# Optimization experiments

Measured on AMD Instinct MI355X. Metric: run time of the kernel, lower is better.

Reference implementation:

```python
import jax, jax.numpy as jnp
import numpy as np

S_CUR, S_MEM, B, D, DFF, L, H = 4096, 16384, 1, 256, 2048, 4, 1
EPS = 1e-5


def _ln(x, w, b):
    mu = x.mean(-1, keepdims=True)
    var = ((x - mu) ** 2).mean(-1, keepdims=True)
    return (x - mu) * jax.lax.rsqrt(var + EPS) * w + b


def _mha(q_in, k_in, v_in, w_qkv, b_qkv, w_o, b_o):
    # torch nn.MultiheadAttention convention: y = x @ W.T + b
    q = q_in @ w_qkv[0].T + b_qkv[0]
    k = k_in @ w_qkv[1].T + b_qkv[1]
    v = v_in @ w_qkv[2].T + b_qkv[2]
    Bq, Sq, _ = q.shape
    Sk = k.shape[1]
    hd = D // H
    q = q.reshape(Bq, Sq, H, hd)
    k = k.reshape(Bq, Sk, H, hd)
    v = v.reshape(Bq, Sk, H, hd)
    scores = jnp.einsum('bqhd,bkhd->bhqk', q, k) / jnp.sqrt(jnp.asarray(hd, q.dtype))
    attn = jax.nn.softmax(scores, axis=-1)
    out = jnp.einsum('bhqk,bkhd->bqhd', attn, v).reshape(Bq, Sq, D)
    return out @ w_o.T + b_o


def setup_inputs() -> dict:
    key = jax.random.key(0)
    ks = jax.random.split(key, 20)
    p = lambda i, shape: 0.02 * jax.random.normal(ks[i], shape, dtype=jnp.float32)
    return {
        'curr': jax.random.normal(ks[0], (S_CUR, B, D), jnp.float32),
        'memory': jax.random.normal(ks[1], (S_MEM, B, D), jnp.float32),
        'curr_pos': jax.random.normal(ks[2], (S_CUR, B, D), jnp.float32),
        'memory_pos': jax.random.normal(ks[3], (S_MEM, B, D), jnp.float32),
        'sa_w_qkv': p(4, (L, 3, D, D)), 'sa_b_qkv': p(5, (L, 3, D)),
        'sa_w_o': p(6, (L, D, D)), 'sa_b_o': p(7, (L, D)),
        'ca_w_qkv': p(8, (L, 3, D, D)), 'ca_b_qkv': p(9, (L, 3, D)),
        'ca_w_o': p(10, (L, D, D)), 'ca_b_o': p(11, (L, D)),
        'ln1_w': jnp.ones((L, D)), 'ln1_b': jnp.zeros((L, D)),
        'ln2_w': jnp.ones((L, D)), 'ln2_b': jnp.zeros((L, D)),
        'ln3_w': jnp.ones((L, D)), 'ln3_b': jnp.zeros((L, D)),
        'mlp_w1': p(12, (L, DFF, D)), 'mlp_b1': p(13, (L, DFF)),
        'mlp_w2': p(14, (L, D, DFF)), 'mlp_b2': p(15, (L, D)),
        'norm_w': jnp.ones((D,)), 'norm_b': jnp.zeros((D,)),
    }


def reference(curr, memory, curr_pos, memory_pos,
              sa_w_qkv, sa_b_qkv, sa_w_o, sa_b_o,
              ca_w_qkv, ca_b_qkv, ca_w_o, ca_b_o,
              ln1_w, ln1_b, ln2_w, ln2_b, ln3_w, ln3_b,
              mlp_w1, mlp_b1, mlp_w2, mlp_b2, norm_w, norm_b):
    # pos_enc_at_input: output = curr + 0.1 * curr_pos (seq-first (S, B, D))
    x = curr + 0.1 * curr_pos
    # batch_first: transpose to (B, S, D) for the layers
    x = jnp.transpose(x, (1, 0, 2))
    mem = jnp.transpose(memory, (1, 0, 2))
    mem_k = mem + jnp.transpose(memory_pos, (1, 0, 2))  # pos added to cross-attn keys
    for l in range(L):
        # pre-norm self-attention (no query_pos at self-attn in SAM2 default)
        t2 = _ln(x, ln1_w[l], ln1_b[l])
        x = x + _mha(t2, t2, t2, sa_w_qkv[l], sa_b_qkv[l], sa_w_o[l], sa_b_o[l])
        # pre-norm cross-attention to memory (keys carry memory_pos, values do not)
        t2 = _ln(x, ln2_w[l], ln2_b[l])
        x = x + _mha(t2, mem_k, mem, ca_w_qkv[l], ca_b_qkv[l], ca_w_o[l], ca_b_o[l])
        # pre-norm ReLU MLP
        t2 = _ln(x, ln3_w[l], ln3_b[l])
        x = x + jax.nn.relu(t2 @ mlp_w1[l].T + mlp_b1[l]) @ mlp_w2[l].T + mlp_b2[l]
    out = _ln(x, norm_w, norm_b)
    return jnp.transpose(out, (1, 0, 2))  # back to (S, B, D)
```

## Files before the change

### kernel.cpp

```cpp
#include <hip/hip_runtime.h>
#include <hip/hip_bf16.h>

typedef unsigned short u16;
typedef unsigned int u32;
typedef __attribute__((ext_vector_type(8))) __bf16 bf16x8;
typedef __attribute__((ext_vector_type(4))) float f32x4;
typedef __attribute__((ext_vector_type(4))) u16 u16x4;
typedef __attribute__((ext_vector_type(8))) u16 u16x8;

#define SCUR 4096
#define SMEM 16384
#define DM   256
#define DFFN 2048
#define NL   4

__device__ __forceinline__ u16 f2b(float f){
  u32 i; __builtin_memcpy(&i, &f, 4);
  u32 r = (i + 0x7fffu + ((i >> 16) & 1u)) >> 16;
  return (u16)r;
}
__device__ __forceinline__ float b2f(u16 v){
  u32 i = ((u32)v) << 16; float f; __builtin_memcpy(&f, &i, 4); return f;
}

__device__ __forceinline__ f32x4 mfma16(bf16x8 a, bf16x8 b, f32x4 c){
  return __builtin_amdgcn_mfma_f32_16x16x32_bf16(a, b, c, 0, 0, 0);
}

__device__ __forceinline__ void glds16(const u16* g, u16* l){
  __builtin_amdgcn_global_load_lds(
      (const __attribute__((address_space(1))) u32*)g,
      (__attribute__((address_space(3))) u32*)l, 16, 0, 0);
}


__global__ void axpy_k(const float* __restrict__ a, const float* __restrict__ b,
                       float s, float* __restrict__ o, int n4){
  int i = blockIdx.x * blockDim.x + threadIdx.x;
  int st = gridDim.x * blockDim.x;
  for (; i < n4; i += st){
    float4 x = ((const float4*)a)[i];
    float4 y = ((const float4*)b)[i];
    float4 r; r.x = x.x + s*y.x; r.y = x.y + s*y.y; r.z = x.z + s*y.z; r.w = x.w + s*y.w;
    ((float4*)o)[i] = r;
  }
}

__global__ void cvt_bf16_k(const float* __restrict__ a, const float* __restrict__ b,
                           u16* __restrict__ o, int n4, float s){
  int i = blockIdx.x * blockDim.x + threadIdx.x;
  int st = gridDim.x * blockDim.x;
  const bool hb = (b != nullptr);
  for (; i < n4; i += st){
    float4 x = ((const float4*)a)[i];
    if (hb){
      float4 y = ((const float4*)b)[i];
      x.x += s*y.x; x.y += s*y.y; x.z += s*y.z; x.w += s*y.w;
    }
    u16x4 r = { f2b(x.x), f2b(x.y), f2b(x.z), f2b(x.w) };
    ((u16x4*)o)[i] = r;
  }
}

template<int OUTF32>
__global__ __launch_bounds__(256) void ln_k(const float* __restrict__ X,
    const float* __restrict__ g, const float* __restrict__ b,
    void* __restrict__ out, int rows){
  int row = blockIdx.x * 4 + (threadIdx.x >> 6);
  int lane = threadIdx.x & 63;
  if (row >= rows) return;
  const float4 v = *(const float4*)(X + (size_t)row*DM + lane*4);
  float s = v.x + v.y + v.z + v.w;
  for (int off = 1; off < 64; off <<= 1) s += __shfl_xor(s, off, 64);
  float mu = s * (1.f/256.f);
  float dx = v.x-mu, dy = v.y-mu, dz = v.z-mu, dw = v.w-mu;
  float q = dx*dx + dy*dy + dz*dz + dw*dw;
  for (int off = 1; off < 64; off <<= 1) q += __shfl_xor(q, off, 64);
  float rstd = rsqrtf(q * (1.f/256.f) + 1e-5f);
  const float4 gw = *(const float4*)(g + lane*4);
  const float4 gb = *(const float4*)(b + lane*4);
  float y0 = dx*rstd*gw.x + gb.x;
  float y1 = dy*rstd*gw.y + gb.y;
  float y2 = dz*rstd*gw.z + gb.z;
  float y3 = dw*rstd*gw.w + gb.w;
  if (OUTF32){
    float4 o; o.x=y0; o.y=y1; o.z=y2; o.w=y3;
    *(float4*)((float*)out + (size_t)row*DM + lane*4) = o;
  } else {
    u16x4 o = { f2b(y0), f2b(y1), f2b(y2), f2b(y3) };
    *(u16x4*)((u16*)out + (size_t)row*DM + lane*4) = o;
  }
}

template<int EPI>
__global__ __launch_bounds__(256) void gemm_bt(
    const u16* __restrict__ A, int lda, const u16* __restrict__ W, int ldw,
    const float* __restrict__ bias, void* __restrict__ out, int ldc,
    int M, int N, int K){
  __shared__ u16 a_sm[64*40];
  __shared__ u16 b_sm[64*40];
  const int tid = threadIdx.x;
  const int lane = tid & 63;
  const int w = tid >> 6;
  const int l16 = lane & 15, lg = lane >> 4;
  const int m0 = blockIdx.y * 64;
  const int n0 = blockIdx.x * 64;
  const int wr = (w >> 1) * 32, wc = (w & 1) * 32;
  f32x4 acc[2][2] = {};
  const int srow = tid >> 2, sch = tid & 3;
  const u16* Ag = A + (size_t)(m0 + srow) * lda + sch * 8;
  const u16* Wg = W + (size_t)(n0 + srow) * ldw + sch * 8;
  u16x8 av = *(const u16x8*)(Ag);
  u16x8 wv = *(const u16x8*)(Wg);
  for (int k0 = 0; k0 < K; k0 += 32){
    __syncthreads();
    *(u16x8*)(a_sm + srow*40 + sch*8) = av;
    *(u16x8*)(b_sm + srow*40 + sch*8) = wv;
    if (k0 + 32 < K){
      av = *(const u16x8*)(Ag + k0 + 32);
      wv = *(const u16x8*)(Wg + k0 + 32);
    }
    __syncthreads();
    bf16x8 af0 = *(const bf16x8*)(a_sm + (wr      + l16)*40 + lg*8);
    bf16x8 af1 = *(const bf16x8*)(a_sm + (wr + 16 + l16)*40 + lg*8);
    bf16x8 bf0 = *(const bf16x8*)(b_sm + (wc      + l16)*40 + lg*8);
    bf16x8 bf1 = *(const bf16x8*)(b_sm + (wc + 16 + l16)*40 + lg*8);
    acc[0][0] = mfma16(af0, bf0, acc[0][0]);
    acc[0][1] = mfma16(af0, bf1, acc[0][1]);
    acc[1][0] = mfma16(af1, bf0, acc[1][0]);
    acc[1][1] = mfma16(af1, bf1, acc[1][1]);
  }
  for (int mi = 0; mi < 2; mi++)
    for (int ni = 0; ni < 2; ni++)
      for (int r = 0; r < 4; r++){
        int m = m0 + wr + mi*16 + lg*4 + r;
        int n = n0 + wc + ni*16 + l16;
        float v = acc[mi][ni][r];
        if (EPI == 3)      v += bias[m];
        else if (EPI != 4) v += bias[n];
        if (EPI == 2)      ((float*)out)[(size_t)m*ldc + n] += v;
        else if (EPI == 1) ((u16*)out)[(size_t)m*ldc + n] = f2b(v > 0.f ? v : 0.f);
        else               ((u16*)out)[(size_t)m*ldc + n] = f2b(v);
      }
}

template<int EPI>
__global__ void gemm128(
    const u16* __restrict__ A, int lda, const u16* __restrict__ W, int ldw,
    const float* __restrict__ bias, void* __restrict__ out, int ldc,
    int M, int N, int K){
  __shared__ u16 a_sm[2][128*32];
  __shared__ u16 b_sm[2][128*32];
  const int tid = threadIdx.x, lane = tid & 63, w = tid >> 6;
  const int l16 = lane & 15, lg = lane >> 4;
  const int m0 = blockIdx.y * 128, n0 = blockIdx.x * 128;
  const int wr = (w >> 1) * 64, wc = (w & 1) * 64;
  f32x4 acc[4][4] = {};
  const int c0 = w*64 + lane, c1 = c0 + 256;
  const int r0 = c0 >> 2, cc0 = c0 & 3;
  const int r1 = c1 >> 2, cc1 = c1 & 3;
  const u16* Ag0 = A + (size_t)(m0 + r0)*lda + cc0*8;
  const u16* Ag1 = A + (size_t)(m0 + r1)*lda + cc1*8;
  const u16* Wg0 = W + (size_t)(n0 + r0)*ldw + cc0*8;
  const u16* Wg1 = W + (size_t)(n0 + r1)*ldw + cc1*8;
  const int nk = K >> 5;
  glds16(Ag0, a_sm[0] + w*512);
  glds16(Ag1, a_sm[0] + w*512 + 2048);
  glds16(Wg0, b_sm[0] + w*512);
  glds16(Wg1, b_sm[0] + w*512 + 2048);
  __builtin_amdgcn_sched_barrier(0);
  for (int k = 0; k < nk; k++){
    const int cur = k & 1;
    if (k + 1 < nk){
      const int nxt = cur ^ 1;
      const int ko = (k + 1) * 32;
      glds16(Ag0 + ko, a_sm[nxt] + w*512);
      glds16(Ag1 + ko, a_sm[nxt] + w*512 + 2048);
      glds16(Wg0 + ko, b_sm[nxt] + w*512);
      glds16(Wg1 + ko, b_sm[nxt] + w*512 + 2048);
      __builtin_amdgcn_sched_barrier(0);
      asm volatile("s_waitcnt vmcnt(4)" ::: "memory");
    } else {
      asm volatile("s_waitcnt vmcnt(0)" ::: "memory");
    }
    __builtin_amdgcn_s_barrier();
    bf16x8 af[4], bf[4];
    #pragma unroll
    for (int mi = 0; mi < 4; mi++)
      af[mi] = *(const bf16x8*)(a_sm[cur] + (wr + mi*16 + l16)*32 + lg*8);
    #pragma unroll
    for (int ni = 0; ni < 4; ni++)
      bf[ni] = *(const bf16x8*)(b_sm[cur] + (wc + ni*16 + l16)*32 + lg*8);
    #pragma unroll
    for (int mi = 0; mi < 4; mi++)
      #pragma unroll
      for (int ni = 0; ni < 4; ni++)
        acc[mi][ni] = mfma16(af[mi], bf[ni], acc[mi][ni]);
    __builtin_amdgcn_s_barrier();
  }
  #pragma unroll
  for (int mi = 0; mi < 4; mi++)
    #pragma unroll
    for (int ni = 0; ni < 4; ni++)
      #pragma unroll
      for (int r = 0; r < 4; r++){
        int m = m0 + wr + mi*16 + lg*4 + r;
        int n = n0 + wc + ni*16 + l16;
        float v = acc[mi][ni][r];
        if (EPI == 1){
          v += bias[n];
          ((u16*)out)[(size_t)m*ldc + n] = f2b(v > 0.f ? v : 0.f);
        } else {
          ((u16*)out)[(size_t)m*ldc + n] = f2b(v);
        }
      }
}

template<int EXPA>
__global__ __launch_bounds__(256) void gemm_pv(
    const u16* __restrict__ A, int lda, const u16* __restrict__ W, int ldw,
    u16* __restrict__ out, int M, int K,
    float* __restrict__ lpart, float scale){
  __shared__ u16 a_sm[64*40];
  __shared__ u16 b_sm[256*40];
  const int tid = threadIdx.x, lane = tid & 63, w = tid >> 6;
  const int l16 = lane & 15, lg = lane >> 4;
  const int m0 = blockIdx.x * 64;
  const int koff = blockIdx.y * K;
  f32x4 acc[4][4] = {};
  const int srow = tid >> 2, sch = tid & 3;
  float lsum = 0.f;
  const u16* Ag = A + (size_t)(m0 + srow) * lda + sch * 8 + koff;
  const u16* Wg = W + (size_t)srow * ldw + sch * 8 + koff;
  u16x8 avX = *(const u16x8*)(Ag);
  u16x8 wv0X = *(const u16x8*)(Wg);
  u16x8 wv1X = *(const u16x8*)(Wg + (size_t)64*ldw);
  u16x8 wv2X = *(const u16x8*)(Wg + (size_t)128*ldw);
  u16x8 wv3X = *(const u16x8*)(Wg + (size_t)192*ldw);
  u16x8 avY = *(const u16x8*)(Ag + 32);
  u16x8 wv0Y = *(const u16x8*)(Wg + 32);
  u16x8 wv1Y = *(const u16x8*)(Wg + (size_t)64*ldw + 32);
  u16x8 wv2Y = *(const u16x8*)(Wg + (size_t)128*ldw + 32);
  u16x8 wv3Y = *(const u16x8*)(Wg + (size_t)192*ldw + 32);
  for (int k0 = 0; k0 < K; k0 += 64){
    u16x8 as;
    if (EXPA){
      #pragma unroll
      for (int e = 0; e < 8; e++){
        float p = __expf(b2f(avX[e]) * scale);
        lsum += p;
        as[e] = f2b(p);
      }
    } else as = avX;
    __syncthreads();
    *(u16x8*)(a_sm + srow*40 + sch*8) = as;
    *(u16x8*)(b_sm + srow*40 + sch*8) = wv0X;
    *(u16x8*)(b_sm + (srow+64)*40 + sch*8) = wv1X;
    *(u16x8*)(b_sm + (srow+128)*40 + sch*8) = wv2X;
    *(u16x8*)(b_sm + (srow+192)*40 + sch*8) = wv3X;
    if (k0 + 64 < K){
      avX  = *(const u16x8*)(Ag + k0 + 64);
      wv0X = *(const u16x8*)(Wg + k0 + 64);
      wv1X = *(const u16x8*)(Wg + (size_t)64*ldw + k0 + 64);
      wv2X = *(const u16x8*)(Wg + (size_t)128*ldw + k0 + 64);
      wv3X = *(const u16x8*)(Wg + (size_t)192*ldw + k0 + 64);
    }
    __syncthreads();
    {
      bf16x8 af[4], bf[4];
      #pragma unroll
      for (int i = 0; i < 4; i++)
        af[i] = *(const bf16x8*)(a_sm + (i*16 + l16)*40 + lg*8);
      #pragma unroll
      for (int i = 0; i < 4; i++)
        bf[i] = *(const bf16x8*)(b_sm + (w*64 + i*16 + l16)*40 + lg*8);
      #pragma unroll
      for (int mi = 0; mi < 4; mi++)
        #pragma unroll
        for (int ni = 0; ni < 4; ni++)
          acc[mi][ni] = mfma16(af[mi], bf[ni], acc[mi][ni]);
    }
    if (EXPA){
      #pragma unroll
      for (int e = 0; e < 8; e++){
        float p = __expf(b2f(avY[e]) * scale);
        lsum += p;
        as[e] = f2b(p);
      }
    } else as = avY;
    __syncthreads();
    *(u16x8*)(a_sm + srow*40 + sch*8) = as;
    *(u16x8*)(b_sm + srow*40 + sch*8) = wv0Y;
    *(u16x8*)(b_sm + (srow+64)*40 + sch*8) = wv1Y;
    *(u16x8*)(b_sm + (srow+128)*40 + sch*8) = wv2Y;
    *(u16x8*)(b_sm + (srow+192)*40 + sch*8) = wv3Y;
    if (k0 + 96 < K){
      avY  = *(const u16x8*)(Ag + k0 + 96);
      wv0Y = *(const u16x8*)(Wg + k0 + 96);
      wv1Y = *(const u16x8*)(Wg + (size_t)64*ldw + k0 + 96);
      wv2Y = *(const u16x8*)(Wg + (size_t)128*ldw + k0 + 96);
      wv3Y = *(const u16x8*)(Wg + (size_t)192*ldw + k0 + 96);
    }
    __syncthreads();
    {
      bf16x8 af[4], bf[4];
      #pragma unroll
      for (int i = 0; i < 4; i++)
        af[i] = *(const bf16x8*)(a_sm + (i*16 + l16)*40 + lg*8);
      #pragma unroll
      for (int i = 0; i < 4; i++)
        bf[i] = *(const bf16x8*)(b_sm + (w*64 + i*16 + l16)*40 + lg*8);
      #pragma unroll
      for (int mi = 0; mi < 4; mi++)
        #pragma unroll
        for (int ni = 0; ni < 4; ni++)
          acc[mi][ni] = mfma16(af[mi], bf[ni], acc[mi][ni]);
    }
  }
  if (EXPA){
    lsum += __shfl_xor(lsum, 1, 64);
    lsum += __shfl_xor(lsum, 2, 64);
    if (sch == 0) lpart[(size_t)blockIdx.y * M + m0 + srow] = lsum;
  }
  u16* op = out + (size_t)blockIdx.y * M * 256;
  #pragma unroll
  for (int mi = 0; mi < 4; mi++)
    #pragma unroll
    for (int ni = 0; ni < 4; ni++)
      #pragma unroll
      for (int r = 0; r < 4; r++){
        int m = m0 + mi*16 + lg*4 + r;
        int n = w*64 + ni*16 + l16;
        op[(size_t)m*256 + n] = f2b(acc[mi][ni][r]);
      }
}

__global__ __launch_bounds__(256) void reduce_pv_k(const u16* __restrict__ P,
    const float* __restrict__ lpart, u16* __restrict__ O, int M, int ks){
  int m = blockIdx.x, d = threadIdx.x;
  const size_t st = (size_t)M * 256;
  float s = 0.f, l = 0.f;
  for (int i = 0; i < ks; i++){
    s += b2f(P[(size_t)i*st + (size_t)m*256 + d]);
    l += lpart[(size_t)i*M + m];
  }
  O[(size_t)m*256 + d] = f2b(s / l);
}
__global__ __launch_bounds__(256) void reduce_res_k(const u16* __restrict__ P,
    const float* __restrict__ bias, float* __restrict__ X, int M, int ks){
  int m = blockIdx.x, d = threadIdx.x;
  const size_t st = (size_t)M * 256;
  float s = bias[d];
  for (int i = 0; i < ks; i++) s += b2f(P[(size_t)i*st + (size_t)m*256 + d]);
  X[(size_t)m*256 + d] += s;
}

extern "C" void kernel_launch(void* const* d_in, const int* in_sizes, int n_in,
                              void* d_out, int out_size, void* d_ws, size_t ws_size,
                              hipStream_t stream){
  (void)in_sizes; (void)n_in; (void)out_size;
  const float* curr       = (const float*)d_in[0];
  const float* memory     = (const float*)d_in[1];
  const float* curr_pos   = (const float*)d_in[2];
  const float* memory_pos = (const float*)d_in[3];
  const float* sa_w_qkv   = (const float*)d_in[4];
  const float* sa_b_qkv   = (const float*)d_in[5];
  const float* sa_w_o     = (const float*)d_in[6];
  const float* sa_b_o     = (const float*)d_in[7];
  const float* ca_w_qkv   = (const float*)d_in[8];
  const float* ca_b_qkv   = (const float*)d_in[9];
  const float* ca_w_o     = (const float*)d_in[10];
  const float* ca_b_o     = (const float*)d_in[11];
  const float* ln1_w = (const float*)d_in[12];
  const float* ln1_b = (const float*)d_in[13];
  const float* ln2_w = (const float*)d_in[14];
  const float* ln2_b = (const float*)d_in[15];
  const float* ln3_w = (const float*)d_in[16];
  const float* ln3_b = (const float*)d_in[17];
  const float* mlp_w1 = (const float*)d_in[18];
  const float* mlp_b1 = (const float*)d_in[19];
  const float* mlp_w2 = (const float*)d_in[20];
  const float* mlp_b2 = (const float*)d_in[21];
  const float* norm_w = (const float*)d_in[22];
  const float* norm_b = (const float*)d_in[23];

  char* wsp = (char*)d_ws;
  auto alloc = [&](size_t bytes)->void*{
    void* r = (void*)wsp; wsp += (bytes + 255) & ~(size_t)255; return r;
  };
  float* x     = (float*)alloc((size_t)SCUR*DM*4);
  u16*   t2b   = (u16*)  alloc((size_t)SCUR*DM*2);
  u16*   qkb   = (u16*)  alloc((size_t)SCUR*2*DM*2);
  u16*   vtsb  = (u16*)  alloc((size_t)DM*SCUR*2);
  u16*   Kb    = (u16*)  alloc((size_t)SMEM*DM*2);
  u16*   vtcb  = (u16*)  alloc((size_t)DM*SMEM*2);
  u16*   memkb = (u16*)  alloc((size_t)SMEM*DM*2);
  u16*   memb  = (u16*)  alloc((size_t)SMEM*DM*2);
  u16*   Hb    = (u16*)  alloc((size_t)SCUR*DFFN*2);
  u16*   Ppart = (u16*)  alloc((size_t)8*SCUR*DM*2);
  float* lpart = (float*)alloc((size_t)16*SCUR*4);
  u16* wb_sa_qkv = (u16*)alloc((size_t)NL*3*DM*DM*2);
  u16* wb_sa_o   = (u16*)alloc((size_t)NL*DM*DM*2);
  u16* wb_ca_qkv = (u16*)alloc((size_t)NL*3*DM*DM*2);
  u16* wb_ca_o   = (u16*)alloc((size_t)NL*DM*DM*2);
  u16* wb_m1     = (u16*)alloc((size_t)NL*DFFN*DM*2);
  u16* wb_m2     = (u16*)alloc((size_t)NL*DM*DFFN*2);

  size_t used  = (size_t)(wsp - (char*)d_ws);
  size_t avail = (ws_size > used) ? (ws_size - used) : 0;
  const size_t rowb = (size_t)SMEM * 2;
  u16* Sbuf;
  int CHc;
  if (avail >= (size_t)SCUR * rowb){
    CHc = SCUR;
    Sbuf = (u16*)alloc((size_t)SCUR * rowb);
  } else {
    size_t ch = (avail / rowb) & ~(size_t)127;
    if (ch >= 512){
      CHc = (int)(ch > SCUR ? SCUR : ch);
      Sbuf = (u16*)alloc((size_t)CHc * rowb);
    } else {
      CHc = 512;
      Sbuf = Hb;
    }
  }
  size_t scap = (size_t)CHc * rowb;
  int CHs = (int)(scap / ((size_t)SCUR*2));
  if (CHs > SCUR) CHs = SCUR;
  CHs &= ~127;
  if (CHs < 128) CHs = 128;

  u16* PVc; int ksc;
  if (Sbuf != Hb){ PVc = Hb; ksc = 16; }
  else           { PVc = Ppart; ksc = 8; }

  u16* Ob = t2b;
  u16* Qb = qkb;

  const float* nullf = nullptr;
  float* nulll = nullptr;
  const float sc = 0.0625f;

  axpy_k<<<dim3(512), dim3(256), 0, stream>>>(curr, curr_pos, 0.1f, x, SCUR*DM/4);
  cvt_bf16_k<<<dim3(1024), dim3(256), 0, stream>>>(memory, memory_pos, memkb, SMEM*DM/4, 1.0f);
  cvt_bf16_k<<<dim3(1024), dim3(256), 0, stream>>>(memory, nullf, memb, SMEM*DM/4, 0.f);
  cvt_bf16_k<<<dim3(512), dim3(256), 0, stream>>>(sa_w_qkv, nullf, wb_sa_qkv, NL*3*DM*DM/4, 0.f);
  cvt_bf16_k<<<dim3(256), dim3(256), 0, stream>>>(sa_w_o,   nullf, wb_sa_o,   NL*DM*DM/4,   0.f);
  cvt_bf16_k<<<dim3(512), dim3(256), 0, stream>>>(ca_w_qkv, nullf, wb_ca_qkv, NL*3*DM*DM/4, 0.f);
  cvt_bf16_k<<<dim3(256), dim3(256), 0, stream>>>(ca_w_o,   nullf, wb_ca_o,   NL*DM*DM/4,   0.f);
  cvt_bf16_k<<<dim3(1024), dim3(256), 0, stream>>>(mlp_w1,  nullf, wb_m1,     NL*DFFN*DM/4, 0.f);
  cvt_bf16_k<<<dim3(1024), dim3(256), 0, stream>>>(mlp_w2,  nullf, wb_m2,     NL*DM*DFFN/4, 0.f);

  const dim3 blk(256);
  for (int l = 0; l < NL; l++){
    ln_k<0><<<dim3(SCUR/4), blk, 0, stream>>>(x, ln1_w + l*DM, ln1_b + l*DM, (void*)t2b, SCUR);
    gemm_bt<0><<<dim3(512/64, SCUR/64), blk, 0, stream>>>(t2b, DM, wb_sa_qkv + (size_t)l*3*DM*DM, DM,
        sa_b_qkv + (size_t)l*3*DM, (void*)qkb, 512, SCUR, 512, DM);
    gemm_bt<3><<<dim3(SCUR/64, DM/64), blk, 0, stream>>>(wb_sa_qkv + ((size_t)l*3+2)*DM*DM, DM, t2b, DM,
        sa_b_qkv + (size_t)l*3*DM + 2*DM, (void*)vtsb, SCUR, DM, SCUR, DM);
    for (int c = 0; c < SCUR; c += CHs){
      int Mc = (SCUR - c) < CHs ? (SCUR - c) : CHs;
      gemm128<4><<<dim3(SCUR/128, Mc/128), blk, 0, stream>>>(qkb + (size_t)c*512, 512, qkb + DM, 512,
          nullf, (void*)Sbuf, SCUR, Mc, SCUR, DM);
      gemm_pv<1><<<dim3(Mc/64, 8), blk, 0, stream>>>(Sbuf, SCUR, vtsb, SCUR,
          Ppart, Mc, SCUR/8, lpart, sc);
      reduce_pv_k<<<dim3(Mc), blk, 0, stream>>>(Ppart, lpart, Ob + (size_t)c*DM, Mc, 8);
    }
    gemm_bt<2><<<dim3(DM/64, SCUR/64), blk, 0, stream>>>(Ob, DM, wb_sa_o + (size_t)l*DM*DM, DM,
        sa_b_o + l*DM, (void*)x, DM, SCUR, DM, DM);

    ln_k<0><<<dim3(SCUR/4), blk, 0, stream>>>(x, ln2_w + l*DM, ln2_b + l*DM, (void*)t2b, SCUR);
    gemm_bt<0><<<dim3(DM/64, SCUR/64), blk, 0, stream>>>(t2b, DM, wb_ca_qkv + ((size_t)l*3+0)*DM*DM, DM,
        ca_b_qkv + l*3*DM + 0*DM, (void*)Qb, DM, SCUR, DM, DM);
    gemm_bt<0><<<dim3(DM/64, SMEM/64), blk, 0, stream>>>(memkb, DM, wb_ca_qkv + ((size_t)l*3+1)*DM*DM, DM,
        ca_b_qkv + l*3*DM + 1*DM, (void*)Kb, DM, SMEM, DM, DM);
    gemm_bt<3><<<dim3(SMEM/64, DM/64), blk, 0, stream>>>(wb_ca_qkv + ((size_t)l*3+2)*DM*DM, DM, memb, DM,
        ca_b_qkv + (size_t)l*3*DM + 2*DM, (void*)vtcb, SMEM, DM, SMEM, DM);
    for (int c = 0; c < SCUR; c += CHc){
      int Mc = (SCUR - c) < CHc ? (SCUR - c) : CHc;
      gemm128<4><<<dim3(SMEM/128, Mc/128), blk, 0, stream>>>(Qb + (size_t)c*DM, DM, Kb, DM,
          nullf, (void*)Sbuf, SMEM, Mc, SMEM, DM);
      gemm_pv<1><<<dim3(Mc/64, ksc), blk, 0, stream>>>(Sbuf, SMEM, vtcb, SMEM,
          PVc, Mc, SMEM/ksc, lpart, sc);
      reduce_pv_k<<<dim3(Mc), blk, 0, stream>>>(PVc, lpart, Ob + (size_t)c*DM, Mc, ksc);
    }
    gemm_bt<2><<<dim3(DM/64, SCUR/64), blk, 0, stream>>>(Ob, DM, wb_ca_o + (size_t)l*DM*DM, DM,
        ca_b_o + l*DM, (void*)x, DM, SCUR, DM, DM);

    ln_k<0><<<dim3(SCUR/4), blk, 0, stream>>>(x, ln3_w + l*DM, ln3_b + l*DM, (void*)t2b, SCUR);
    gemm128<1><<<dim3(DFFN/128, SCUR/128), blk, 0, stream>>>(t2b, DM, wb_m1 + (size_t)l*DFFN*DM, DM,
        mlp_b1 + l*DFFN, (void*)Hb, DFFN, SCUR, DFFN, DM);
    gemm_pv<0><<<dim3(SCUR/64, 4), blk, 0, stream>>>(Hb, DFFN, wb_m2 + (size_t)l*DM*DFFN, DFFN,
        Ppart, SCUR, DFFN/4, nulll, 0.f);
    reduce_res_k<<<dim3(SCUR), blk, 0, stream>>>(Ppart, mlp_b2 + l*DM, x, SCUR, 4);
  }

  ln_k<1><<<dim3(SCUR/4), blk, 0, stream>>>(x, norm_w, norm_b, d_out, SCUR);
}
```

Before: 1.066 ms.

## Fuse softmax exponentiation and row-sum into score GEMM epilogue

```diff
diff --git a/kernel.cpp b/kernel.cpp
--- a/kernel.cpp
+++ b/kernel.cpp
@@ -148,7 +148,7 @@
 __global__ void gemm128(
     const u16* __restrict__ A, int lda, const u16* __restrict__ W, int ldw,
     const float* __restrict__ bias, void* __restrict__ out, int ldc,
-    int M, int N, int K){
+    int M, int N, int K, float scale, float* __restrict__ lpart){
   __shared__ u16 a_sm[2][128*32];
   __shared__ u16 b_sm[2][128*32];
   const int tid = threadIdx.x, lane = tid & 63, w = tid >> 6;
@@ -198,6 +198,26 @@
         acc[mi][ni] = mfma16(af[mi], bf[ni], acc[mi][ni]);
     __builtin_amdgcn_s_barrier();
   }
+  if (EPI == 6){
+    #pragma unroll
+    for (int mi = 0; mi < 4; mi++)
+      #pragma unroll
+      for (int r = 0; r < 4; r++){
+        float ls = 0.f;
+        #pragma unroll
+        for (int ni = 0; ni < 4; ni++){
+          float p = __expf(acc[mi][ni][r] * scale);
+          acc[mi][ni][r] = p;
+          ls += p;
+        }
+        #pragma unroll
+        for (int off = 1; off < 16; off <<= 1) ls += __shfl_xor(ls, off, 64);
+        if (l16 == 0){
+          int m = m0 + wr + mi*16 + lg*4 + r;
+          lpart[(size_t)(blockIdx.x*2 + (w & 1)) * M + m] = ls;
+        }
+      }
+  }
   #pragma unroll
   for (int mi = 0; mi < 4; mi++)
     #pragma unroll
@@ -216,11 +236,9 @@
       }
 }
 
-template<int EXPA>
 __global__ __launch_bounds__(256) void gemm_pv(
     const u16* __restrict__ A, int lda, const u16* __restrict__ W, int ldw,
-    u16* __restrict__ out, int M, int K,
-    float* __restrict__ lpart, float scale){
+    u16* __restrict__ out, int M, int K){
   __shared__ u16 a_sm[64*40];
   __shared__ u16 b_sm[256*40];
   const int tid = threadIdx.x, lane = tid & 63, w = tid >> 6;
@@ -229,7 +247,6 @@
   const int koff = blockIdx.y * K;
   f32x4 acc[4][4] = {};
   const int srow = tid >> 2, sch = tid & 3;
-  float lsum = 0.f;
   const u16* Ag = A + (size_t)(m0 + srow) * lda + sch * 8 + koff;
   const u16* Wg = W + (size_t)srow * ldw + sch * 8 + koff;
   u16x8 avX = *(const u16x8*)(Ag);
@@ -243,17 +260,8 @@
   u16x8 wv2Y = *(const u16x8*)(Wg + (size_t)128*ldw + 32);
   u16x8 wv3Y = *(const u16x8*)(Wg + (size_t)192*ldw + 32);
   for (int k0 = 0; k0 < K; k0 += 64){
-    u16x8 as;
-    if (EXPA){
-      #pragma unroll
-      for (int e = 0; e < 8; e++){
-        float p = __expf(b2f(avX[e]) * scale);
-        lsum += p;
-        as[e] = f2b(p);
-      }
-    } else as = avX;
-    __syncthreads();
-    *(u16x8*)(a_sm + srow*40 + sch*8) = as;
+    __syncthreads();
+    *(u16x8*)(a_sm + srow*40 + sch*8) = avX;
     *(u16x8*)(b_sm + srow*40 + sch*8) = wv0X;
     *(u16x8*)(b_sm + (srow+64)*40 + sch*8) = wv1X;
     *(u16x8*)(b_sm + (srow+128)*40 + sch*8) = wv2X;
@@ -280,16 +288,8 @@
         for (int ni = 0; ni < 4; ni++)
           acc[mi][ni] = mfma16(af[mi], bf[ni], acc[mi][ni]);
     }
-    if (EXPA){
-      #pragma unroll
-      for (int e = 0; e < 8; e++){
-        float p = __expf(b2f(avY[e]) * scale);
-        lsum += p;
-        as[e] = f2b(p);
-      }
-    } else as = avY;
-    __syncthreads();
-    *(u16x8*)(a_sm + srow*40 + sch*8) = as;
+    __syncthreads();
+    *(u16x8*)(a_sm + srow*40 + sch*8) = avY;
     *(u16x8*)(b_sm + srow*40 + sch*8) = wv0Y;
     *(u16x8*)(b_sm + (srow+64)*40 + sch*8) = wv1Y;
     *(u16x8*)(b_sm + (srow+128)*40 + sch*8) = wv2Y;
@@ -317,11 +317,6 @@
           acc[mi][ni] = mfma16(af[mi], bf[ni], acc[mi][ni]);
     }
   }
-  if (EXPA){
-    lsum += __shfl_xor(lsum, 1, 64);
-    lsum += __shfl_xor(lsum, 2, 64);
-    if (sch == 0) lpart[(size_t)blockIdx.y * M + m0 + srow] = lsum;
-  }
   u16* op = out + (size_t)blockIdx.y * M * 256;
   #pragma unroll
   for (int mi = 0; mi < 4; mi++)
@@ -336,14 +331,20 @@
 }
 
 __global__ __launch_bounds__(256) void reduce_pv_k(const u16* __restrict__ P,
-    const float* __restrict__ lpart, u16* __restrict__ O, int M, int ks){
+    const float* __restrict__ lpart, u16* __restrict__ O, int M, int ks, int nlp){
+  __shared__ float lred[4];
   int m = blockIdx.x, d = threadIdx.x;
+  int lane = d & 63, w = d >> 6;
+  float la = 0.f;
+  for (int i = d; i < nlp; i += 256) la += lpart[(size_t)i*M + m];
+  #pragma unroll
+  for (int off = 1; off < 64; off <<= 1) la += __shfl_xor(la, off, 64);
+  if (lane == 0) lred[w] = la;
+  __syncthreads();
+  float l = lred[0] + lred[1] + lred[2] + lred[3];
   const size_t st = (size_t)M * 256;
-  float s = 0.f, l = 0.f;
-  for (int i = 0; i < ks; i++){
-    s += b2f(P[(size_t)i*st + (size_t)m*256 + d]);
-    l += lpart[(size_t)i*M + m];
-  }
+  float s = 0.f;
+  for (int i = 0; i < ks; i++) s += b2f(P[(size_t)i*st + (size_t)m*256 + d]);
   O[(size_t)m*256 + d] = f2b(s / l);
 }
 __global__ __launch_bounds__(256) void reduce_res_k(const u16* __restrict__ P,
@@ -398,7 +399,7 @@
   u16*   memb  = (u16*)  alloc((size_t)SMEM*DM*2);
   u16*   Hb    = (u16*)  alloc((size_t)SCUR*DFFN*2);
   u16*   Ppart = (u16*)  alloc((size_t)8*SCUR*DM*2);
-  float* lpart = (float*)alloc((size_t)16*SCUR*4);
+  float* lpart = (float*)alloc((size_t)256*SCUR*4);
   u16* wb_sa_qkv = (u16*)alloc((size_t)NL*3*DM*DM*2);
   u16* wb_sa_o   = (u16*)alloc((size_t)NL*DM*DM*2);
   u16* wb_ca_qkv = (u16*)alloc((size_t)NL*3*DM*DM*2);
@@ -460,11 +461,10 @@
         sa_b_qkv + (size_t)l*3*DM + 2*DM, (void*)vtsb, SCUR, DM, SCUR, DM);
     for (int c = 0; c < SCUR; c += CHs){
       int Mc = (SCUR - c) < CHs ? (SCUR - c) : CHs;
-      gemm128<4><<<dim3(SCUR/128, Mc/128), blk, 0, stream>>>(qkb + (size_t)c*512, 512, qkb + DM, 512,
-          nullf, (void*)Sbuf, SCUR, Mc, SCUR, DM);
-      gemm_pv<1><<<dim3(Mc/64, 8), blk, 0, stream>>>(Sbuf, SCUR, vtsb, SCUR,
-          Ppart, Mc, SCUR/8, lpart, sc);
-      reduce_pv_k<<<dim3(Mc), blk, 0, stream>>>(Ppart, lpart, Ob + (size_t)c*DM, Mc, 8);
+      gemm128<6><<<dim3(SCUR/128, Mc/128), blk, 0, stream>>>(qkb + (size_t)c*512, 512, qkb + DM, 512,
+          nullf, (void*)Sbuf, SCUR, Mc, SCUR, DM, sc, lpart);
+      gemm_pv<<<dim3(Mc/64, 8), blk, 0, stream>>>(Sbuf, SCUR, vtsb, SCUR, Ppart, Mc, SCUR/8);
+      reduce_pv_k<<<dim3(Mc), blk, 0, stream>>>(Ppart, lpart, Ob + (size_t)c*DM, Mc, 8, (SCUR/128)*2);
     }
     gemm_bt<2><<<dim3(DM/64, SCUR/64), blk, 0, stream>>>(Ob, DM, wb_sa_o + (size_t)l*DM*DM, DM,
         sa_b_o + l*DM, (void*)x, DM, SCUR, DM, DM);
@@ -478,20 +478,19 @@
         ca_b_qkv + (size_t)l*3*DM + 2*DM, (void*)vtcb, SMEM, DM, SMEM, DM);
     for (int c = 0; c < SCUR; c += CHc){
       int Mc = (SCUR - c) < CHc ? (SCUR - c) : CHc;
-      gemm128<4><<<dim3(SMEM/128, Mc/128), blk, 0, stream>>>(Qb + (size_t)c*DM, DM, Kb, DM,
-          nullf, (void*)Sbuf, SMEM, Mc, SMEM, DM);
-      gemm_pv<1><<<dim3(Mc/64, ksc), blk, 0, stream>>>(Sbuf, SMEM, vtcb, SMEM,
-          PVc, Mc, SMEM/ksc, lpart, sc);
-      reduce_pv_k<<<dim3(Mc), blk, 0, stream>>>(PVc, lpart, Ob + (size_t)c*DM, Mc, ksc);
+      gemm128<6><<<dim3(SMEM/128, Mc/128), blk, 0, stream>>>(Qb + (size_t)c*DM, DM, Kb, DM,
+          nullf, (void*)Sbuf, SMEM, Mc, SMEM, DM, sc, lpart);
+      gemm_pv<<<dim3(Mc/64, ksc), blk, 0, stream>>>(Sbuf, SMEM, vtcb, SMEM, PVc, Mc, SMEM/ksc);
+      reduce_pv_k<<<dim3(Mc), blk, 0, stream>>>(PVc, lpart, Ob + (size_t)c*DM, Mc, ksc, (SMEM/128)*2);
     }
     gemm_bt<2><<<dim3(DM/64, SCUR/64), blk, 0, stream>>>(Ob, DM, wb_ca_o + (size_t)l*DM*DM, DM,
         ca_b_o + l*DM, (void*)x, DM, SCUR, DM, DM);
 
     ln_k<0><<<dim3(SCUR/4), blk, 0, stream>>>(x, ln3_w + l*DM, ln3_b + l*DM, (void*)t2b, SCUR);
     gemm128<1><<<dim3(DFFN/128, SCUR/128), blk, 0, stream>>>(t2b, DM, wb_m1 + (size_t)l*DFFN*DM, DM,
-        mlp_b1 + l*DFFN, (void*)Hb, DFFN, SCUR, DFFN, DM);
-    gemm_pv<0><<<dim3(SCUR/64, 4), blk, 0, stream>>>(Hb, DFFN, wb_m2 + (size_t)l*DM*DFFN, DFFN,
-        Ppart, SCUR, DFFN/4, nulll, 0.f);
+        mlp_b1 + l*DFFN, (void*)Hb, DFFN, SCUR, DFFN, DM, 0.f, nulll);
+    gemm_pv<<<dim3(SCUR/64, 4), blk, 0, stream>>>(Hb, DFFN, wb_m2 + (size_t)l*DM*DFFN, DFFN,
+        Ppart, SCUR, DFFN/4);
     reduce_res_k<<<dim3(SCUR), blk, 0, stream>>>(Ppart, mlp_b2 + l*DM, x, SCUR, 4);
   }
 
```

Result: slower. 1.124 ms (+5.5%).
